# Performance work log

Measured on AMD Instinct MI355X. Metric: run time of the kernel, lower is better.

The kernel has to match this reference:

```python
import jax, jax.numpy as jnp
import numpy as np

N_E, N_U, N_D = 512, 256, 256
N_A = 16
N_FB = 4
N_SV = 256
N_PV = 64
D_IN0 = 3 * (4 * N_A) + 2 * 4   # 200, fb_block output at layer 0
D_IN = 3 * N_SV + 2 * N_PV      # 896, fb_block output thereafter


def _fb_block(s_v, p_v):
    # s_v: (n_e, d_s); p_v: (n_e, n_e, d_p)
    n_e = N_U + N_D
    su_m = jnp.tile(s_v[:N_U].mean(0)[None, :], (n_e, 1))
    sd_m = jnp.tile(s_v[N_U:].mean(0)[None, :], (n_e, 1))
    pu_m = p_v[:N_U].mean(0)   # (n_e, d_p)
    pd_m = p_v[N_U:].mean(0)
    return jnp.concatenate([su_m, sd_m, pu_m, pd_m, s_v], axis=-1)


def setup_inputs() -> dict:
    key = jax.random.key(0)
    ks = jax.random.split(key, 16)

    def lin(k, fin, fout):
        k1, k2 = jax.random.split(k)
        lim = 1.0 / np.sqrt(fin)
        W = jax.random.uniform(k1, (fin, fout), minval=-lim, maxval=lim, dtype=jnp.float32)
        b = jax.random.uniform(k2, (fout,), minval=-lim, maxval=lim, dtype=jnp.float32)
        return W, b

    V0_W, V0_b = lin(ks[0], D_IN0, N_SV)
    W0_W, W0_b = lin(ks[1], 4, N_PV)
    VrW, Vrb, WrW, Wrb = [], [], [], []
    for i in range(N_FB - 1):
        w, b = lin(ks[2 + i], D_IN, N_SV); VrW.append(w); Vrb.append(b)
        w, b = lin(ks[6 + i], N_PV, N_PV); WrW.append(w); Wrb.append(b)
    Vr_W, Vr_b = jnp.stack(VrW), jnp.stack(Vrb)
    Wr_W, Wr_b = jnp.stack(WrW), jnp.stack(Wrb)
    Vhu_W, Vhu_b = lin(ks[10], D_IN, N_SV)
    Vhd_W, Vhd_b = lin(ks[11], D_IN, N_SV)
    wu_W, wu_b = lin(ks[12], N_SV, N_U)
    wd_W, wd_b = lin(ks[13], N_SV, N_D)
    r = jax.random.normal(ks[14], (N_E, 3), dtype=jnp.float32)
    a = jax.random.normal(ks[15], (N_A, 3), dtype=jnp.float32) * 2.0
    return dict(r=r, a=a, V0_W=V0_W, V0_b=V0_b, Vr_W=Vr_W, Vr_b=Vr_b,
                W0_W=W0_W, W0_b=W0_b, Wr_W=Wr_W, Wr_b=Wr_b,
                Vhu_W=Vhu_W, Vhu_b=Vhu_b, Vhd_W=Vhd_W, Vhd_b=Vhd_b,
                wu_W=wu_W, wu_b=wu_b, wd_W=wd_W, wd_b=wd_b)


def reference(r, a, V0_W, V0_b, Vr_W, Vr_b, W0_W, W0_b, Wr_W, Wr_b,
              Vhu_W, Vhu_b, Vhd_W, Vhd_b, wu_W, wu_b, wd_W, wd_b):
    n_e = N_E
    eye = jnp.eye(n_e, dtype=r.dtype)[:, :, None]
    ra = r[:, None, :] - a[None, :, :]                       # (n_e, n_a, 3)
    ra_len = jnp.linalg.norm(ra, axis=-1, keepdims=True)
    rr = r[None, :, :] - r[:, None, :]                       # (n_e, n_e, 3)
    rr_len = jnp.linalg.norm(rr + eye, axis=-1, keepdims=True)
    s_v = jnp.concatenate([ra, ra_len], axis=-1).reshape(n_e, -1)   # (n_e, 4*n_a)
    p_v = jnp.concatenate([rr, rr_len], axis=-1)                    # (n_e, n_e, 4)
    s_blk = _fb_block(s_v, p_v)
    for l in range(N_FB):
        VW, Vb = (V0_W, V0_b) if l == 0 else (Vr_W[l - 1], Vr_b[l - 1])
        WW, Wb = (W0_W, W0_b) if l == 0 else (Wr_W[l - 1], Wr_b[l - 1])
        s_new = jnp.tanh(s_blk @ VW + Vb)
        s_v = s_new + s_v if s_v.shape[-1] == N_SV else s_new   # residual skips layer 0
        p_new = jnp.tanh(p_v @ WW + Wb)
        p_v = p_new + p_v if p_v.shape[-1] == N_PV else p_new
        s_blk = _fb_block(s_v, p_v)
    s_u = jnp.tanh(s_blk[:N_U] @ Vhu_W + Vhu_b)
    s_d = jnp.tanh(s_blk[N_U:] @ Vhd_W + Vhd_b)
    s_wu = s_u @ wu_W + wu_b                                  # (n_u, n_u)
    s_wd = s_d @ wd_W + wd_b                                  # (n_d, n_d)
    exp_u = jnp.linalg.norm(ra[:N_U], axis=-1, keepdims=True)  # (n_u, n_a, 1)
    exp_d = jnp.linalg.norm(ra[N_U:], axis=-1, keepdims=True)
    orb_u = (s_wu * jnp.exp(-exp_u).sum(axis=1))[None]         # (1, n_u, n_u)
    orb_d = (s_wd * jnp.exp(-exp_d).sum(axis=1))[None]
    # logabssumdet with n_det == 1, matrix dim > 1
    sgn_u, log_u = jnp.linalg.slogdet(orb_u)
    sgn_d, log_d = jnp.linalg.slogdet(orb_d)
    psi = (sgn_u * sgn_d * jnp.exp(log_u + log_d)).sum()
    return jnp.log(jnp.abs(psi))
```

## Files before the change

### kernel.cpp

```cpp
#include <hip/hip_runtime.h>
#include <hip/hip_bf16.h>

#define NE 512

__device__ __align__(16) float g_sv0[NE*64];
__device__ __align__(16) float g_sv[2][NE*256];
__device__ __align__(16) float g_pu4[NE*4];
__device__ __align__(16) float g_pd4[NE*4];
__device__ __align__(16) float g_puL[4*NE*64];
__device__ __align__(16) float g_pdL[4*NE*64];
__device__ __align__(16) float g_su0[64];
__device__ __align__(16) float g_sd0[64];
__device__ __align__(16) float g_su[256];
__device__ __align__(16) float g_sd[256];
__device__ __align__(16) float g_part4[4*16*NE*64];
__device__ __align__(16) float g_f[NE];
__device__ __align__(16) float g_hu[256*256];
__device__ __align__(16) float g_hd[256*256];
__device__ __align__(16) float g_orbu[256*256];
__device__ __align__(16) float g_orbd[256*256];
__device__ float g_logs[2];

__device__ __forceinline__ float tanh_fast(float x) {
  float e = __expf(2.f * x);
  return 1.f - 2.f / (e + 1.f);
}

__global__ __launch_bounds__(256, 2) void k_front(const float* __restrict__ r,
                                                  const float* __restrict__ a,
                                                  const float* __restrict__ W0,
                                                  const float* __restrict__ b0,
                                                  const float* __restrict__ Wr,
                                                  const float* __restrict__ brs) {
  __shared__ __align__(16) float xrow[4*32*68];
  __shared__ __align__(16) float wtile[4096];
  __shared__ __align__(16) float msc[4*4*68];
  __shared__ float red[4][4];
  int bid = blockIdx.x, t = threadIdx.x;
  if (bid < 512) {
    int j = bid;
    if (j == 0) {
      for (int h = 0; h < 2; ++h) {
        int e = h*256 + t;
        float rx = r[3*e], ry = r[3*e+1], rz = r[3*e+2];
        float facc = 0.f;
        #pragma unroll
        for (int at = 0; at < 16; ++at) {
          float dx = rx - a[3*at], dy = ry - a[3*at+1], dz = rz - a[3*at+2];
          float len = sqrtf(dx*dx + dy*dy + dz*dz);
          g_sv0[e*64 + 4*at + 0] = dx;
          g_sv0[e*64 + 4*at + 1] = dy;
          g_sv0[e*64 + 4*at + 2] = dz;
          g_sv0[e*64 + 4*at + 3] = len;
          facc += expf(-len);
        }
        g_f[e] = facc;
      }
      __syncthreads();
      if (t < 128) {
        int h = t >> 6, c = t & 63;
        float s = 0.f;
        for (int i = 0; i < 256; ++i) s += g_sv0[(h*256 + i)*64 + c];
        (h ? g_sd0 : g_su0)[c] = s * (1.f/256.f);
      }
      __syncthreads();
    }
    float rjx = r[3*j], rjy = r[3*j+1], rjz = r[3*j+2];
    for (int h = 0; h < 2; ++h) {
      int i = h*256 + t;
      float dx = rjx - r[3*i], dy = rjy - r[3*i+1], dz = rjz - r[3*i+2];
      float ee = (i == j) ? 1.f : 0.f;
      float ex = dx+ee, ey = dy+ee, ez = dz+ee;
      float len = sqrtf(ex*ex + ey*ey + ez*ez);
      float v0 = dx, v1 = dy, v2 = dz, v3 = len;
      #pragma unroll
      for (int m = 1; m < 64; m <<= 1) {
        v0 += __shfl_xor(v0, m); v1 += __shfl_xor(v1, m);
        v2 += __shfl_xor(v2, m); v3 += __shfl_xor(v3, m);
      }
      if ((t & 63) == 0) {
        int wv = t >> 6;
        red[wv][0]=v0; red[wv][1]=v1; red[wv][2]=v2; red[wv][3]=v3;
      }
      __syncthreads();
      if (t == 0) {
        float* dst = h ? g_pd4 : g_pu4;
        #pragma unroll
        for (int c = 0; c < 4; ++c)
          dst[j*4 + c] = (red[0][c]+red[1][c]+red[2][c]+red[3][c]) * (1.f/256.f);
      }
      __syncthreads();
    }
  } else {
    int lane = t & 63, wv = t >> 6;
    int gw = (bid - 512)*4 + wv;
    int j = gw >> 4, chunk = gw & 15;
    int i0 = chunk * 32;
    int rg = lane >> 4, cg = lane & 15;
    float* xr = xrow + wv*(32*68);
    float* ms = msc + wv*(4*68);
    float rjx = r[3*j], rjy = r[3*j+1], rjz = r[3*j+2];
    float xres[8][4];
    {
      float4 w0 = *(const float4*)&W0[0*64 + 4*cg];
      float4 w1 = *(const float4*)&W0[1*64 + 4*cg];
      float4 w2 = *(const float4*)&W0[2*64 + 4*cg];
      float4 w3 = *(const float4*)&W0[3*64 + 4*cg];
      float4 bv = *(const float4*)&b0[4*cg];
      #pragma unroll
      for (int q = 0; q < 8; ++q) {
        int row = 4*q + rg;
        int i = i0 + row;
        float dx = rjx - r[3*i], dy = rjy - r[3*i+1], dz = rjz - r[3*i+2];
        float ee = (i == j) ? 1.f : 0.f;
        float ex = dx+ee, ey = dy+ee, ez = dz+ee;
        float len = sqrtf(ex*ex + ey*ey + ez*ez);
        float y0 = tanh_fast(bv.x + dx*w0.x + dy*w1.x + dz*w2.x + len*w3.x);
        float y1 = tanh_fast(bv.y + dx*w0.y + dy*w1.y + dz*w2.y + len*w3.y);
        float y2 = tanh_fast(bv.z + dx*w0.z + dy*w1.z + dz*w2.z + len*w3.z);
        float y3 = tanh_fast(bv.w + dx*w0.w + dy*w1.w + dz*w2.w + len*w3.w);
        xres[q][0]=y0; xres[q][1]=y1; xres[q][2]=y2; xres[q][3]=y3;
        float4 yv; yv.x=y0; yv.y=y1; yv.z=y2; yv.w=y3;
        *(float4*)&xr[row*68 + 4*cg] = yv;
      }
      float cs0=0,cs1=0,cs2=0,cs3=0;
      #pragma unroll
      for (int q=0;q<8;++q){cs0+=xres[q][0];cs1+=xres[q][1];cs2+=xres[q][2];cs3+=xres[q][3];}
      ms[rg*68+4*cg+0]=cs0; ms[rg*68+4*cg+1]=cs1;
      ms[rg*68+4*cg+2]=cs2; ms[rg*68+4*cg+3]=cs3;
      float tot = ms[0*68+lane]+ms[1*68+lane]+ms[2*68+lane]+ms[3*68+lane];
      g_part4[0*(16*NE*64) + chunk*(NE*64) + j*64 + lane] = tot;
    }
    for (int l = 0; l < 3; ++l) {
      __syncthreads();
      for (int idx = t; idx < 4096; idx += 256) wtile[idx] = Wr[l*4096 + idx];
      __syncthreads();
      float4 bv = *(const float4*)&brs[l*64 + 4*cg];
      float acc[8][4];
      #pragma unroll
      for (int q=0;q<8;++q){acc[q][0]=bv.x;acc[q][1]=bv.y;acc[q][2]=bv.z;acc[q][3]=bv.w;}
      #pragma unroll 4
      for (int kq = 0; kq < 16; ++kq) {
        float4 wv0 = *(const float4*)&wtile[(4*kq+0)*64 + 4*cg];
        float4 wv1 = *(const float4*)&wtile[(4*kq+1)*64 + 4*cg];
        float4 wv2 = *(const float4*)&wtile[(4*kq+2)*64 + 4*cg];
        float4 wv3 = *(const float4*)&wtile[(4*kq+3)*64 + 4*cg];
        #pragma unroll
        for (int q = 0; q < 8; ++q) {
          float4 xv = *(const float4*)&xr[(4*q+rg)*68 + 4*kq];
          acc[q][0] += xv.x*wv0.x + xv.y*wv1.x + xv.z*wv2.x + xv.w*wv3.x;
          acc[q][1] += xv.x*wv0.y + xv.y*wv1.y + xv.z*wv2.y + xv.w*wv3.y;
          acc[q][2] += xv.x*wv0.z + xv.y*wv1.z + xv.z*wv2.z + xv.w*wv3.z;
          acc[q][3] += xv.x*wv0.w + xv.y*wv1.w + xv.z*wv2.w + xv.w*wv3.w;
        }
      }
      float cs0=0,cs1=0,cs2=0,cs3=0;
      #pragma unroll
      for (int q = 0; q < 8; ++q) {
        float y0 = tanh_fast(acc[q][0]) + xres[q][0];
        float y1 = tanh_fast(acc[q][1]) + xres[q][1];
        float y2 = tanh_fast(acc[q][2]) + xres[q][2];
        float y3 = tanh_fast(acc[q][3]) + xres[q][3];
        xres[q][0]=y0; xres[q][1]=y1; xres[q][2]=y2; xres[q][3]=y3;
        float4 yv; yv.x=y0; yv.y=y1; yv.z=y2; yv.w=y3;
        *(float4*)&xr[(4*q+rg)*68 + 4*cg] = yv;
        cs0+=y0; cs1+=y1; cs2+=y2; cs3+=y3;
      }
      ms[rg*68+4*cg+0]=cs0; ms[rg*68+4*cg+1]=cs1;
      ms[rg*68+4*cg+2]=cs2; ms[rg*68+4*cg+3]=cs3;
      float tot = ms[0*68+lane]+ms[1*68+lane]+ms[2*68+lane]+ms[3*68+lane];
      g_part4[(l+1)*(16*NE*64) + chunk*(NE*64) + j*64 + lane] = tot;
    }
  }
}

__global__ __launch_bounds__(256) void k_reduce_p() {
  int idx = blockIdx.x*256 + threadIdx.x;
  int l = idx >> 16;
  int rem = idx & 65535;
  int half = rem >> 15;
  int r2 = rem & 32767;
  int j = r2 >> 6, c = r2 & 63;
  const float* pp = g_part4 + l*(16*NE*64) + half*(8*NE*64) + j*64 + c;
  float s = 0.f;
  #pragma unroll
  for (int ch = 0; ch < 8; ++ch) s += pp[ch*(NE*64)];
  (half ? g_pdL : g_puL)[l*(NE*64) + j*64 + c] = s * (1.f/256.f);
}

__global__ __launch_bounds__(256) void k_smean(int svsel) {
  int h = blockIdx.x, t = threadIdx.x;
  const float* sv = g_sv[svsel];
  float s = 0.f;
  for (int i = 0; i < 256; ++i) s += sv[(h*256 + i)*256 + t];
  (h ? g_sd : g_su)[t] = s * (1.f/256.f);
}

template<int PUK, int SVK, int MEANK>
__global__ __launch_bounds__(256) void k_smm(int which, const float* __restrict__ W,
                                             const float* __restrict__ Wb,
                                             const float* __restrict__ W2,
                                             const float* __restrict__ Wb2,
                                             int pl) {
  constexpr int MAINK = 2*PUK + SVK;
  __shared__ __align__(16) float wsl[MAINK*32];
  __shared__ float insl[32*(MAINK+1)];
  __shared__ float biasv[32];
  __shared__ float bred[256];
  const float *pu_p=nullptr, *pd_p=nullptr, *sv_p=nullptr, *su_p=nullptr, *sd_p=nullptr;
  const float *res_p=nullptr, *rs_p=nullptr;
  float* out_p = nullptr;
  int t = threadIdx.x;
  int rg = blockIdx.x, cg = blockIdx.y;
  int grp = 0, rgl = rg;
  if (which >= 4) { grp = rg >> 3; rgl = rg & 7; }
  const float* Wsel = (which >= 4 && grp) ? W2 : W;
  const float* Wbsel = (which >= 4 && grp) ? Wb2 : Wb;
  int in_base = 0, dotanh = 1;
  switch (which) {
    case 0: pu_p=g_pu4; pd_p=g_pd4; su_p=g_su0; sd_p=g_sd0; sv_p=g_sv0;
            out_p=g_sv[0]; in_base=rg*32; break;
    case 1: case 2: case 3:
      pu_p=g_puL + pl*(NE*64); pd_p=g_pdL + pl*(NE*64); su_p=g_su; sd_p=g_sd;
      sv_p=g_sv[(which+1)&1]; res_p=sv_p; out_p=g_sv[which&1]; in_base=rg*32; break;
    case 4: pu_p=g_puL + pl*(NE*64); pd_p=g_pdL + pl*(NE*64); su_p=g_su; sd_p=g_sd;
            sv_p=g_sv[1]; out_p = grp ? g_hd : g_hu; in_base = grp*256 + rgl*32; break;
    default: sv_p = grp ? g_hd : g_hu; out_p = grp ? g_orbd : g_orbu;
             rs_p = g_f + grp*256; in_base = rgl*32; dotanh = 0; break;
  }
  int out_base = (which >= 4) ? rgl*32 : rg*32;
  int col0 = cg * 32;
  for (int idx = t; idx < MAINK*32; idx += 256) {
    int c = idx >> 5, cl = idx & 31;
    wsl[idx] = Wsel[(2*MEANK + c)*256 + col0 + cl];
  }
  for (int rr = 0; rr < 32; ++rr) {
    int row = in_base + rr;
    for (int c = t; c < MAINK; c += 256) {
      float v;
      if (c < PUK) v = pu_p[row*PUK + c];
      else if (c < 2*PUK) v = pd_p[row*PUK + (c - PUK)];
      else v = sv_p[row*SVK + (c - 2*PUK)];
      insl[rr*(MAINK+1) + c] = v;
    }
  }
  {
    int pcol = t & 31, ps = t >> 5;
    float bacc = 0.f;
    if (MEANK > 0) {
      for (int c = ps; c < MEANK; c += 8)
        bacc += su_p[c]*Wsel[c*256 + col0 + pcol] + sd_p[c]*Wsel[(MEANK + c)*256 + col0 + pcol];
    }
    bred[ps*32 + pcol] = bacc;
  }
  __syncthreads();
  if (t < 32) {
    float s = Wbsel[col0 + t];
    #pragma unroll
    for (int p8 = 0; p8 < 8; ++p8) s += bred[p8*32 + t];
    biasv[t] = s;
  }
  __syncthreads();
  int c4 = t & 7, rl = t >> 3;
  float a0 = biasv[4*c4], a1 = biasv[4*c4+1], a2 = biasv[4*c4+2], a3 = biasv[4*c4+3];
  const float* inrow = &insl[rl*(MAINK+1)];
  #pragma unroll 4
  for (int c = 0; c < MAINK; ++c) {
    float iv = inrow[c];
    float4 wv = *(const float4*)&wsl[c*32 + 4*c4];
    a0 += iv*wv.x; a1 += iv*wv.y; a2 += iv*wv.z; a3 += iv*wv.w;
  }
  int rowA = out_base + rl;
  int col = col0 + 4*c4;
  if (dotanh) { a0=tanh_fast(a0); a1=tanh_fast(a1); a2=tanh_fast(a2); a3=tanh_fast(a3); }
  if (res_p) {
    float4 rv = *(const float4*)&res_p[rowA*256 + col];
    a0 += rv.x; a1 += rv.y; a2 += rv.z; a3 += rv.w;
  }
  if (rs_p) { float fsc = rs_p[rowA]; a0*=fsc; a1*=fsc; a2*=fsc; a3*=fsc; }
  float4 ov; ov.x=a0; ov.y=a1; ov.z=a2; ov.w=a3;
  *(float4*)&out_p[rowA*256 + col] = ov;
}

#define REP8(M) M(0) M(1) M(2) M(3) M(4) M(5) M(6) M(7)
#define DPPMAX(v, CTRL) { unsigned _o = (unsigned)__builtin_amdgcn_update_dpp(0, (int)(v), CTRL, 0xf, 0xf, true); \
                          (v) = (v) > _o ? (v) : _o; }

__global__ __launch_bounds__(512, 2) void k_lu() {
  __shared__ __align__(16) float colbuf[2][256];
  __shared__ __align__(16) float prowbuf[2][16*20];
  const float* A = (blockIdx.x == 0) ? g_orbu : g_orbd;
  int t = threadIdx.x;
  int tile_c = t >> 5;
  int tile_r = t & 31;
  int lane = t & 63;
  int br = tile_r * 8;
  int pb = tile_c * 20;
  const float4* Ap = (const float4*)(A + br*256 + tile_c*16);
#define DECLROW(R) float4 M##R##_0 = Ap[R*64+0], M##R##_1 = Ap[R*64+1], \
                          M##R##_2 = Ap[R*64+2], M##R##_3 = Ap[R*64+3];
  REP8(DECLROW)
#undef DECLROW
  unsigned um = 0;
  if (tile_c == 0) {
#define INIT0(R) colbuf[0][br+R] = M##R##_0.x;
    REP8(INIT0)
#undef INIT0
  }
  __syncthreads();
  float prod = 1.f;
  int esum = 0;
  float m0=0,m1=0,m2=0,m3=0,m4=0,m5=0,m6=0,m7=0;
  for (int k = 0; k < 256; ++k) {
    const float* cbin = colbuf[k & 1];
    float4 cv = *(const float4*)&cbin[4*lane];
    float4 ca = *(const float4*)&cbin[br];
    float4 cb2 = *(const float4*)&cbin[br+4];
    bool aliveU = (tile_c*16 + 15) >= k;
    if (k > 0 && aliveU) {
      const float* pwp = &prowbuf[(k-1) & 1][pb];
      float4 P0 = *(const float4*)&pwp[0];
      float4 P1 = *(const float4*)&pwp[4];
      float4 P2 = *(const float4*)&pwp[8];
      float4 P3 = *(const float4*)&pwp[12];
#define UPD(R) { float mr = m##R; \
  M##R##_0.x -= mr*P0.x; M##R##_0.y -= mr*P0.y; M##R##_0.z -= mr*P0.z; M##R##_0.w -= mr*P0.w; \
  M##R##_1.x -= mr*P1.x; M##R##_1.y -= mr*P1.y; M##R##_1.z -= mr*P1.z; M##R##_1.w -= mr*P1.w; \
  M##R##_2.x -= mr*P2.x; M##R##_2.y -= mr*P2.y; M##R##_2.z -= mr*P2.z; M##R##_2.w -= mr*P2.w; \
  M##R##_3.x -= mr*P3.x; M##R##_3.y -= mr*P3.y; M##R##_3.z -= mr*P3.z; M##R##_3.w -= mr*P3.w; }
      REP8(UPD)
#undef UPD
    }
    unsigned b0 = (um & 1u) ? 0u : ((__float_as_uint(fabsf(cv.x)) & 0xFFFFFF00u) | (unsigned)(4*lane+0));
    unsigned b1 = (um & 2u) ? 0u : ((__float_as_uint(fabsf(cv.y)) & 0xFFFFFF00u) | (unsigned)(4*lane+1));
    unsigned b2 = (um & 4u) ? 0u : ((__float_as_uint(fabsf(cv.z)) & 0xFFFFFF00u) | (unsigned)(4*lane+2));
    unsigned b3 = (um & 8u) ? 0u : ((__float_as_uint(fabsf(cv.w)) & 0xFFFFFF00u) | (unsigned)(4*lane+3));
    unsigned bb = max(max(b0,b1), max(b2,b3));
    DPPMAX(bb, 0x111) DPPMAX(bb, 0x112) DPPMAX(bb, 0x114) DPPMAX(bb, 0x118)
    DPPMAX(bb, 0x142) DPPMAX(bb, 0x143)
    bb = (unsigned)__builtin_amdgcn_readlane((int)bb, 63);
    int p = (int)(bb & 255u);
    int wl = p >> 2, cc = p & 3;
    unsigned px = (unsigned)__builtin_amdgcn_readlane((int)__float_as_uint(cv.x), wl);
    unsigned py = (unsigned)__builtin_amdgcn_readlane((int)__float_as_uint(cv.y), wl);
    unsigned pz = (unsigned)__builtin_amdgcn_readlane((int)__float_as_uint(cv.z), wl);
    unsigned pw = (unsigned)__builtin_amdgcn_readlane((int)__float_as_uint(cv.w), wl);
    float piv = __uint_as_float(cc==0 ? px : cc==1 ? py : cc==2 ? pz : pw);
    int ee; float mant = frexpf(fabsf(piv), &ee);
    prod *= mant; esum += ee;
    int e2; prod = frexpf(prod, &e2); esum += e2;
    if (wl == lane) um |= 1u << cc;
    if (k == 255) break;
    float rp = 1.0f / piv;
    m0 = ca.x*rp; m1 = ca.y*rp; m2 = ca.z*rp; m3 = ca.w*rp;
    m4 = cb2.x*rp; m5 = cb2.y*rp; m6 = cb2.z*rp; m7 = cb2.w*rp;
    bool aliveK = (tile_c*16 + 15) > k;
    if (aliveK && tile_r == (p >> 3)) {
      float* pw_ = &prowbuf[k & 1][pb];
      switch (p & 7) {
#define PUBC(R) case R: *(float4*)&pw_[0] = M##R##_0; *(float4*)&pw_[4] = M##R##_1; \
                        *(float4*)&pw_[8] = M##R##_2; *(float4*)&pw_[12] = M##R##_3; break;
        REP8(PUBC)
#undef PUBC
      }
    }
    int kn = k + 1;
    if (tile_c == (kn >> 4)) {
      float e0,e1,e2b,e3,e4,e5,e6,e7;
      switch (kn & 15) {
#define EXTC(I, G, C) case I: e0=M0_##G.C; e1=M1_##G.C; e2b=M2_##G.C; e3=M3_##G.C; \
                              e4=M4_##G.C; e5=M5_##G.C; e6=M6_##G.C; e7=M7_##G.C; break;
        EXTC(0,0,x) EXTC(1,0,y) EXTC(2,0,z) EXTC(3,0,w)
        EXTC(4,1,x) EXTC(5,1,y) EXTC(6,1,z) EXTC(7,1,w)
        EXTC(8,2,x) EXTC(9,2,y) EXTC(10,2,z) EXTC(11,2,w)
        EXTC(12,3,x) EXTC(13,3,y) EXTC(14,3,z) EXTC(15,3,w)
#undef EXTC
      }
      float sel;
      switch (p & 7) {
        case 0: sel = e0; break; case 1: sel = e1; break;
        case 2: sel = e2b; break; case 3: sel = e3; break;
        case 4: sel = e4; break; case 5: sel = e5; break;
        case 6: sel = e6; break; default: sel = e7; break;
      }
      float pv = __shfl(sel, (tile_c & 1)*32 + (p >> 3), 64);
      float4 w0, w1;
      w0.x = e0 - m0*pv; w0.y = e1 - m1*pv; w0.z = e2b - m2*pv; w0.w = e3 - m3*pv;
      w1.x = e4 - m4*pv; w1.y = e5 - m5*pv; w1.z = e6 - m6*pv; w1.w = e7 - m7*pv;
      *(float4*)&colbuf[kn & 1][br] = w0;
      *(float4*)&colbuf[kn & 1][br+4] = w1;
    }
    __syncthreads();
  }
  if (t == 0) g_logs[blockIdx.x] = logf(prod) + (float)esum * 0.69314718055994531f;
}

__global__ void k_final(float* out) { out[0] = g_logs[0] + g_logs[1]; }

extern "C" void kernel_launch(void* const* d_in, const int* in_sizes, int n_in,
                              void* d_out, int out_size, void* d_ws, size_t ws_size,
                              hipStream_t stream) {
  const float* r     = (const float*)d_in[0];
  const float* a     = (const float*)d_in[1];
  const float* V0_W  = (const float*)d_in[2];
  const float* V0_b  = (const float*)d_in[3];
  const float* Vr_W  = (const float*)d_in[4];
  const float* Vr_b  = (const float*)d_in[5];
  const float* W0_W  = (const float*)d_in[6];
  const float* W0_b  = (const float*)d_in[7];
  const float* Wr_W  = (const float*)d_in[8];
  const float* Wr_b  = (const float*)d_in[9];
  const float* Vhu_W = (const float*)d_in[10];
  const float* Vhu_b = (const float*)d_in[11];
  const float* Vhd_W = (const float*)d_in[12];
  const float* Vhd_b = (const float*)d_in[13];
  const float* wu_W  = (const float*)d_in[14];
  const float* wu_b  = (const float*)d_in[15];
  const float* wd_W  = (const float*)d_in[16];
  const float* wd_b  = (const float*)d_in[17];
  float* out = (float*)d_out;

  k_front<<<2560, 256, 0, stream>>>(r, a, W0_W, W0_b, Wr_W, Wr_b);
  k_reduce_p<<<1024, 256, 0, stream>>>();

  k_smm<4,64,64><<<dim3(16,8), 256, 0, stream>>>(0, V0_W, V0_b, nullptr, nullptr, 0);
  k_smean<<<2, 256, 0, stream>>>(0);
  k_smm<64,256,256><<<dim3(16,8), 256, 0, stream>>>(1, Vr_W + 0*896*256, Vr_b + 0,
                                                    nullptr, nullptr, 0);
  k_smean<<<2, 256, 0, stream>>>(1);
  k_smm<64,256,256><<<dim3(16,8), 256, 0, stream>>>(2, Vr_W + 1*896*256, Vr_b + 256,
                                                    nullptr, nullptr, 1);
  k_smean<<<2, 256, 0, stream>>>(0);
  k_smm<64,256,256><<<dim3(16,8), 256, 0, stream>>>(3, Vr_W + 2*896*256, Vr_b + 512,
                                                    nullptr, nullptr, 2);
  k_smean<<<2, 256, 0, stream>>>(1);
  k_smm<64,256,256><<<dim3(16,8), 256, 0, stream>>>(4, Vhu_W, Vhu_b, Vhd_W, Vhd_b, 3);
  k_smm<0,256,0><<<dim3(16,8), 256, 0, stream>>>(6, wu_W, wu_b, wd_W, wd_b, 0);
  k_lu<<<2, 512, 0, stream>>>();
  k_final<<<1, 1, 0, stream>>>(out);
}
```

Measured before the change: 641.8 us.

## Fuse mid-stage kernels into one persistent kernel with software grid barriers

Replaces the reduce, smean and smm launches with a single persistent 256-block kernel that moves between stages using an atomic-counter grid barrier. The matmul tiles are halved to 16 rows so 256 blocks fill more CUs, and the K loop is split across two thread halves that reduce through shared memory. The separate final-sum kernel is folded into the LU kernel using an atomic completion counter. This removes many small launches and their gaps, but correctness now depends on all 256 blocks being co-resident, and every barrier spin-waits on global atomics.

```diff
diff --git a/kernel.cpp b/kernel.cpp
--- a/kernel.cpp
+++ b/kernel.cpp
@@ -20,6 +20,8 @@
 __device__ __align__(16) float g_orbu[256*256];
 __device__ __align__(16) float g_orbd[256*256];
 __device__ float g_logs[2];
+__device__ unsigned g_barcnt;
+__device__ unsigned g_ludone;
 
 __device__ __forceinline__ float tanh_fast(float x) {
   float e = __expf(2.f * x);
@@ -37,6 +39,7 @@
   __shared__ __align__(16) float msc[4*4*68];
   __shared__ float red[4][4];
   int bid = blockIdx.x, t = threadIdx.x;
+  if (bid == 0 && t == 0) { g_barcnt = 0u; g_ludone = 0u; }
   if (bid < 512) {
     int j = bid;
     if (j == 0) {
@@ -174,119 +177,181 @@
   }
 }
 
-__global__ __launch_bounds__(256) void k_reduce_p() {
-  int idx = blockIdx.x*256 + threadIdx.x;
-  int l = idx >> 16;
-  int rem = idx & 65535;
-  int half = rem >> 15;
-  int r2 = rem & 32767;
-  int j = r2 >> 6, c = r2 & 63;
-  const float* pp = g_part4 + l*(16*NE*64) + half*(8*NE*64) + j*64 + c;
-  float s = 0.f;
-  #pragma unroll
-  for (int ch = 0; ch < 8; ++ch) s += pp[ch*(NE*64)];
-  (half ? g_pdL : g_puL)[l*(NE*64) + j*64 + c] = s * (1.f/256.f);
-}
-
-__global__ __launch_bounds__(256) void k_smean(int svsel) {
-  int h = blockIdx.x, t = threadIdx.x;
-  const float* sv = g_sv[svsel];
-  float s = 0.f;
-  for (int i = 0; i < 256; ++i) s += sv[(h*256 + i)*256 + t];
-  (h ? g_sd : g_su)[t] = s * (1.f/256.f);
-}
-
-template<int PUK, int SVK, int MEANK>
-__global__ __launch_bounds__(256) void k_smm(int which, const float* __restrict__ W,
-                                             const float* __restrict__ Wb,
-                                             const float* __restrict__ W2,
-                                             const float* __restrict__ Wb2,
-                                             int pl) {
-  constexpr int MAINK = 2*PUK + SVK;
-  __shared__ __align__(16) float wsl[MAINK*32];
-  __shared__ float insl[32*(MAINK+1)];
-  __shared__ float biasv[32];
-  __shared__ float bred[256];
-  const float *pu_p=nullptr, *pd_p=nullptr, *sv_p=nullptr, *su_p=nullptr, *sd_p=nullptr;
-  const float *res_p=nullptr, *rs_p=nullptr;
-  float* out_p = nullptr;
-  int t = threadIdx.x;
-  int rg = blockIdx.x, cg = blockIdx.y;
-  int grp = 0, rgl = rg;
-  if (which >= 4) { grp = rg >> 3; rgl = rg & 7; }
-  const float* Wsel = (which >= 4 && grp) ? W2 : W;
-  const float* Wbsel = (which >= 4 && grp) ? Wb2 : Wb;
-  int in_base = 0, dotanh = 1;
-  switch (which) {
-    case 0: pu_p=g_pu4; pd_p=g_pd4; su_p=g_su0; sd_p=g_sd0; sv_p=g_sv0;
-            out_p=g_sv[0]; in_base=rg*32; break;
-    case 1: case 2: case 3:
-      pu_p=g_puL + pl*(NE*64); pd_p=g_pdL + pl*(NE*64); su_p=g_su; sd_p=g_sd;
-      sv_p=g_sv[(which+1)&1]; res_p=sv_p; out_p=g_sv[which&1]; in_base=rg*32; break;
-    case 4: pu_p=g_puL + pl*(NE*64); pd_p=g_pdL + pl*(NE*64); su_p=g_su; sd_p=g_sd;
-            sv_p=g_sv[1]; out_p = grp ? g_hd : g_hu; in_base = grp*256 + rgl*32; break;
-    default: sv_p = grp ? g_hd : g_hu; out_p = grp ? g_orbd : g_orbu;
-             rs_p = g_f + grp*256; in_base = rgl*32; dotanh = 0; break;
-  }
-  int out_base = (which >= 4) ? rgl*32 : rg*32;
-  int col0 = cg * 32;
+__device__ __forceinline__ void gridbar(int t, int phase) {
+  __syncthreads();
+  if (t == 0) {
+    __hip_atomic_fetch_add(&g_barcnt, 1u, __ATOMIC_ACQ_REL, __HIP_MEMORY_SCOPE_AGENT);
+    unsigned tgt = 256u * (unsigned)phase;
+    while (__hip_atomic_load(&g_barcnt, __ATOMIC_ACQUIRE, __HIP_MEMORY_SCOPE_AGENT) < tgt)
+      __builtin_amdgcn_s_sleep(2);
+  }
+  __syncthreads();
+}
+
+__device__ __forceinline__ void smm_stage(int bid, int t,
+    const float* W, const float* Wb,
+    const float* pu_p, const float* pd_p,
+    const float* su_p, const float* sd_p,
+    const float* sv_p, const float* res_p, const float* rs_p,
+    float* out_p, int PUK, int SVK, int MAINK, int MEANK,
+    int sin_base, int out_base, bool dotanh,
+    float* wsl, float* insl, float* bred, float* biasv, float4* pacc) {
+  int cg = bid & 7, col0 = cg*32;
   for (int idx = t; idx < MAINK*32; idx += 256) {
     int c = idx >> 5, cl = idx & 31;
-    wsl[idx] = Wsel[(2*MEANK + c)*256 + col0 + cl];
-  }
-  for (int rr = 0; rr < 32; ++rr) {
-    int row = in_base + rr;
+    wsl[idx] = W[(2*MEANK + c)*256 + col0 + cl];
+  }
+  for (int rr = 0; rr < 16; ++rr) {
+    int row = sin_base + rr;
     for (int c = t; c < MAINK; c += 256) {
       float v;
       if (c < PUK) v = pu_p[row*PUK + c];
       else if (c < 2*PUK) v = pd_p[row*PUK + (c - PUK)];
       else v = sv_p[row*SVK + (c - 2*PUK)];
-      insl[rr*(MAINK+1) + c] = v;
+      insl[rr*385 + c] = v;
     }
   }
   {
     int pcol = t & 31, ps = t >> 5;
     float bacc = 0.f;
+    for (int c = ps; c < MEANK; c += 8)
+      bacc += su_p[c]*W[c*256 + col0 + pcol] + sd_p[c]*W[(MEANK + c)*256 + col0 + pcol];
+    bred[ps*32 + pcol] = bacc;
+  }
+  __syncthreads();
+  if (t < 32) {
+    float s = Wb[col0 + t];
     if (MEANK > 0) {
-      for (int c = ps; c < MEANK; c += 8)
-        bacc += su_p[c]*Wsel[c*256 + col0 + pcol] + sd_p[c]*Wsel[(MEANK + c)*256 + col0 + pcol];
-    }
-    bred[ps*32 + pcol] = bacc;
-  }
-  __syncthreads();
-  if (t < 32) {
-    float s = Wbsel[col0 + t];
-    #pragma unroll
-    for (int p8 = 0; p8 < 8; ++p8) s += bred[p8*32 + t];
+      #pragma unroll
+      for (int p8 = 0; p8 < 8; ++p8) s += bred[p8*32 + t];
+    }
     biasv[t] = s;
   }
   __syncthreads();
-  int c4 = t & 7, rl = t >> 3;
-  float a0 = biasv[4*c4], a1 = biasv[4*c4+1], a2 = biasv[4*c4+2], a3 = biasv[4*c4+3];
-  const float* inrow = &insl[rl*(MAINK+1)];
+  int kh = t >> 7, tt = t & 127, rl = tt >> 3, c4 = tt & 7;
+  int H = MAINK >> 1, c0 = kh*H;
+  float a0=0.f, a1=0.f, a2=0.f, a3=0.f;
+  const float* inrow = &insl[rl*385];
   #pragma unroll 4
-  for (int c = 0; c < MAINK; ++c) {
+  for (int c = c0; c < c0 + H; ++c) {
     float iv = inrow[c];
     float4 wv = *(const float4*)&wsl[c*32 + 4*c4];
     a0 += iv*wv.x; a1 += iv*wv.y; a2 += iv*wv.z; a3 += iv*wv.w;
   }
-  int rowA = out_base + rl;
-  int col = col0 + 4*c4;
-  if (dotanh) { a0=tanh_fast(a0); a1=tanh_fast(a1); a2=tanh_fast(a2); a3=tanh_fast(a3); }
-  if (res_p) {
-    float4 rv = *(const float4*)&res_p[rowA*256 + col];
-    a0 += rv.x; a1 += rv.y; a2 += rv.z; a3 += rv.w;
-  }
-  if (rs_p) { float fsc = rs_p[rowA]; a0*=fsc; a1*=fsc; a2*=fsc; a3*=fsc; }
-  float4 ov; ov.x=a0; ov.y=a1; ov.z=a2; ov.w=a3;
-  *(float4*)&out_p[rowA*256 + col] = ov;
+  float4 av; av.x=a0; av.y=a1; av.z=a2; av.w=a3;
+  pacc[t] = av;
+  __syncthreads();
+  if (kh == 0) {
+    float4 o = pacc[t + 128];
+    a0 += o.x + biasv[4*c4+0];
+    a1 += o.y + biasv[4*c4+1];
+    a2 += o.z + biasv[4*c4+2];
+    a3 += o.w + biasv[4*c4+3];
+    if (dotanh) { a0=tanh_fast(a0); a1=tanh_fast(a1); a2=tanh_fast(a2); a3=tanh_fast(a3); }
+    int rowA = out_base + rl;
+    int col = col0 + 4*c4;
+    if (res_p) {
+      float4 rv = *(const float4*)&res_p[rowA*256 + col];
+      a0 += rv.x; a1 += rv.y; a2 += rv.z; a3 += rv.w;
+    }
+    if (rs_p) { float fsc = rs_p[rowA]; a0*=fsc; a1*=fsc; a2*=fsc; a3*=fsc; }
+    float4 ov; ov.x=a0; ov.y=a1; ov.z=a2; ov.w=a3;
+    *(float4*)&out_p[rowA*256 + col] = ov;
+  }
+}
+
+__device__ __forceinline__ void smean_stage(int bid, int t, const float* sv, float* bred) {
+  if (bid < 16) {
+    int h = bid & 1, cs = bid >> 1;
+    int pcol = t & 31, rseg = t >> 5;
+    float s = 0.f;
+    for (int i = rseg*32; i < rseg*32 + 32; ++i)
+      s += sv[(h*256 + i)*256 + cs*32 + pcol];
+    bred[rseg*32 + pcol] = s;
+    __syncthreads();
+    if (t < 32) {
+      float tot = 0.f;
+      #pragma unroll
+      for (int r8 = 0; r8 < 8; ++r8) tot += bred[r8*32 + t];
+      (h ? g_sd : g_su)[cs*32 + t] = tot * (1.f/256.f);
+    }
+  }
+}
+
+__global__ __launch_bounds__(256) void k_mid(const float* __restrict__ V0_W,
+                                             const float* __restrict__ V0_b,
+                                             const float* __restrict__ Vr_W,
+                                             const float* __restrict__ Vr_b,
+                                             const float* __restrict__ Vhu_W,
+                                             const float* __restrict__ Vhu_b,
+                                             const float* __restrict__ Vhd_W,
+                                             const float* __restrict__ Vhd_b,
+                                             const float* __restrict__ wu_W,
+                                             const float* __restrict__ wu_b,
+                                             const float* __restrict__ wd_W,
+                                             const float* __restrict__ wd_b) {
+  __shared__ __align__(16) float wsl[384*32];
+  __shared__ __align__(16) float insl[16*385];
+  __shared__ float bred[256];
+  __shared__ float biasv[32];
+  __shared__ __align__(16) float4 pacc[256];
+  int bid = blockIdx.x, t = threadIdx.x;
+  #pragma unroll
+  for (int rep = 0; rep < 4; ++rep) {
+    int idx = rep*65536 + bid*256 + t;
+    int l = idx >> 16;
+    int rem = idx & 65535;
+    int half = rem >> 15;
+    int r2 = rem & 32767;
+    const float* pp = g_part4 + l*(16*NE*64) + half*(8*NE*64) + r2;
+    float s = 0.f;
+    #pragma unroll
+    for (int ch = 0; ch < 8; ++ch) s += pp[ch*(NE*64)];
+    (half ? g_pdL : g_puL)[l*(NE*64) + r2] = s * (1.f/256.f);
+  }
+  gridbar(t, 1);
+  int rg = bid >> 3;
+  int grp = rg >> 4, rgl = rg & 15;
+  smm_stage(bid, t, V0_W, V0_b, g_pu4, g_pd4, g_su0, g_sd0, g_sv0,
+            nullptr, nullptr, g_sv[0], 4, 64, 72, 64, rg*16, rg*16, true,
+            wsl, insl, bred, biasv, pacc);
+  gridbar(t, 2);
+  smean_stage(bid, t, g_sv[0], bred);
+  gridbar(t, 3);
+  smm_stage(bid, t, Vr_W + 0*896*256, Vr_b + 0, g_puL + 0*(NE*64), g_pdL + 0*(NE*64),
+            g_su, g_sd, g_sv[0], g_sv[0], nullptr, g_sv[1], 64, 256, 384, 256,
+            rg*16, rg*16, true, wsl, insl, bred, biasv, pacc);
+  gridbar(t, 4);
+  smean_stage(bid, t, g_sv[1], bred);
+  gridbar(t, 5);
+  smm_stage(bid, t, Vr_W + 1*896*256, Vr_b + 256, g_puL + 1*(NE*64), g_pdL + 1*(NE*64),
+            g_su, g_sd, g_sv[1], g_sv[1], nullptr, g_sv[0], 64, 256, 384, 256,
+            rg*16, rg*16, true, wsl, insl, bred, biasv, pacc);
+  gridbar(t, 6);
+  smean_stage(bid, t, g_sv[0], bred);
+  gridbar(t, 7);
+  smm_stage(bid, t, Vr_W + 2*896*256, Vr_b + 512, g_puL + 2*(NE*64), g_pdL + 2*(NE*64),
+            g_su, g_sd, g_sv[0], g_sv[0], nullptr, g_sv[1], 64, 256, 384, 256,
+            rg*16, rg*16, true, wsl, insl, bred, biasv, pacc);
+  gridbar(t, 8);
+  smean_stage(bid, t, g_sv[1], bred);
+  gridbar(t, 9);
+  smm_stage(bid, t, grp ? Vhd_W : Vhu_W, grp ? Vhd_b : Vhu_b,
+            g_puL + 3*(NE*64), g_pdL + 3*(NE*64), g_su, g_sd, g_sv[1],
+            nullptr, nullptr, grp ? g_hd : g_hu, 64, 256, 384, 256,
+            grp*256 + rgl*16, rgl*16, true, wsl, insl, bred, biasv, pacc);
+  gridbar(t, 10);
+  smm_stage(bid, t, grp ? wd_W : wu_W, grp ? wd_b : wu_b,
+            nullptr, nullptr, nullptr, nullptr, grp ? g_hd : g_hu,
+            nullptr, g_f + grp*256, grp ? g_orbd : g_orbu, 0, 256, 256, 0,
+            rgl*16, rgl*16, false, wsl, insl, bred, biasv, pacc);
 }
 
 #define REP8(M) M(0) M(1) M(2) M(3) M(4) M(5) M(6) M(7)
 #define DPPMAX(v, CTRL) { unsigned _o = (unsigned)__builtin_amdgcn_update_dpp(0, (int)(v), CTRL, 0xf, 0xf, true); \
                           (v) = (v) > _o ? (v) : _o; }
 
-__global__ __launch_bounds__(512, 2) void k_lu() {
+__global__ __launch_bounds__(512, 2) void k_lu(float* __restrict__ out) {
   __shared__ __align__(16) float colbuf[2][256];
   __shared__ __align__(16) float prowbuf[2][16*20];
   const float* A = (blockIdx.x == 0) ? g_orbu : g_orbd;
@@ -392,10 +457,17 @@
     }
     __syncthreads();
   }
-  if (t == 0) g_logs[blockIdx.x] = logf(prod) + (float)esum * 0.69314718055994531f;
-}
-
-__global__ void k_final(float* out) { out[0] = g_logs[0] + g_logs[1]; }
+  if (t == 0) {
+    float ls = logf(prod) + (float)esum * 0.69314718055994531f;
+    __hip_atomic_store(&g_logs[blockIdx.x], ls, __ATOMIC_RELEASE, __HIP_MEMORY_SCOPE_AGENT);
+    unsigned old = __hip_atomic_fetch_add(&g_ludone, 1u, __ATOMIC_ACQ_REL, __HIP_MEMORY_SCOPE_AGENT);
+    if (old == 1u) {
+      float l0 = __hip_atomic_load(&g_logs[0], __ATOMIC_ACQUIRE, __HIP_MEMORY_SCOPE_AGENT);
+      float l1 = __hip_atomic_load(&g_logs[1], __ATOMIC_ACQUIRE, __HIP_MEMORY_SCOPE_AGENT);
+      out[0] = l0 + l1;
+    }
+  }
+}
 
 extern "C" void kernel_launch(void* const* d_in, const int* in_sizes, int n_in,
                               void* d_out, int out_size, void* d_ws, size_t ws_size,
@@ -421,21 +493,7 @@
   float* out = (float*)d_out;
 
   k_front<<<2560, 256, 0, stream>>>(r, a, W0_W, W0_b, Wr_W, Wr_b);
-  k_reduce_p<<<1024, 256, 0, stream>>>();
-
-  k_smm<4,64,64><<<dim3(16,8), 256, 0, stream>>>(0, V0_W, V0_b, nullptr, nullptr, 0);
-  k_smean<<<2, 256, 0, stream>>>(0);
-  k_smm<64,256,256><<<dim3(16,8), 256, 0, stream>>>(1, Vr_W + 0*896*256, Vr_b + 0,
-                                                    nullptr, nullptr, 0);
-  k_smean<<<2, 256, 0, stream>>>(1);
-  k_smm<64,256,256><<<dim3(16,8), 256, 0, stream>>>(2, Vr_W + 1*896*256, Vr_b + 256,
-                                                    nullptr, nullptr, 1);
-  k_smean<<<2, 256, 0, stream>>>(0);
-  k_smm<64,256,256><<<dim3(16,8), 256, 0, stream>>>(3, Vr_W + 2*896*256, Vr_b + 512,
-                                                    nullptr, nullptr, 2);
-  k_smean<<<2, 256, 0, stream>>>(1);
-  k_smm<64,256,256><<<dim3(16,8), 256, 0, stream>>>(4, Vhu_W, Vhu_b, Vhd_W, Vhd_b, 3);
-  k_smm<0,256,0><<<dim3(16,8), 256, 0, stream>>>(6, wu_W, wu_b, wd_W, wd_b, 0);
-  k_lu<<<2, 512, 0, stream>>>();
-  k_final<<<1, 1, 0, stream>>>(out);
-}
+  k_mid<<<256, 256, 0, stream>>>(V0_W, V0_b, Vr_W, Vr_b, Vhu_W, Vhu_b,
+                                 Vhd_W, Vhd_b, wu_W, wu_b, wd_W, wd_b);
+  k_lu<<<2, 512, 0, stream>>>(out);
+}
```

Result: slower. 704.3 us (+9.7%).

## Fuse s-mean reduction into matmul epilogues and fold final sum into LU

Applied to the files above, without the earlier changes.

Removes the separate k_smean kernels. Each k_smm block now writes per-rowgroup column partial sums of its output, and the next layer's k_smm reduces those partials into shared memory before it starts. The k_final launch is also removed: the two LU blocks combine their log values through an atomic counter that is reset in k_front. This cuts several small serial kernel launches, including the 256-iteration column-mean loops, at the cost of a little redundant partial-sum reduction in every block.

```diff
diff --git a/kernel.cpp b/kernel.cpp
--- a/kernel.cpp
+++ b/kernel.cpp
@@ -11,15 +11,15 @@
 __device__ __align__(16) float g_pdL[4*NE*64];
 __device__ __align__(16) float g_su0[64];
 __device__ __align__(16) float g_sd0[64];
-__device__ __align__(16) float g_su[256];
-__device__ __align__(16) float g_sd[256];
 __device__ __align__(16) float g_part4[4*16*NE*64];
+__device__ __align__(16) float g_spart[2][16*256];
 __device__ __align__(16) float g_f[NE];
 __device__ __align__(16) float g_hu[256*256];
 __device__ __align__(16) float g_hd[256*256];
 __device__ __align__(16) float g_orbu[256*256];
 __device__ __align__(16) float g_orbd[256*256];
 __device__ float g_logs[2];
+__device__ unsigned g_ludone;
 
 __device__ __forceinline__ float tanh_fast(float x) {
   float e = __expf(2.f * x);
@@ -37,6 +37,7 @@
   __shared__ __align__(16) float msc[4*4*68];
   __shared__ float red[4][4];
   int bid = blockIdx.x, t = threadIdx.x;
+  if (bid == 0 && t == 0) g_ludone = 0u;
   if (bid < 512) {
     int j = bid;
     if (j == 0) {
@@ -180,20 +181,11 @@
   int rem = idx & 65535;
   int half = rem >> 15;
   int r2 = rem & 32767;
-  int j = r2 >> 6, c = r2 & 63;
-  const float* pp = g_part4 + l*(16*NE*64) + half*(8*NE*64) + j*64 + c;
+  const float* pp = g_part4 + l*(16*NE*64) + half*(8*NE*64) + r2;
   float s = 0.f;
   #pragma unroll
   for (int ch = 0; ch < 8; ++ch) s += pp[ch*(NE*64)];
-  (half ? g_pdL : g_puL)[l*(NE*64) + j*64 + c] = s * (1.f/256.f);
-}
-
-__global__ __launch_bounds__(256) void k_smean(int svsel) {
-  int h = blockIdx.x, t = threadIdx.x;
-  const float* sv = g_sv[svsel];
-  float s = 0.f;
-  for (int i = 0; i < 256; ++i) s += sv[(h*256 + i)*256 + t];
-  (h ? g_sd : g_su)[t] = s * (1.f/256.f);
+  (half ? g_pdL : g_puL)[l*(NE*64) + r2] = s * (1.f/256.f);
 }
 
 template<int PUK, int SVK, int MEANK>
@@ -201,12 +193,14 @@
                                              const float* __restrict__ Wb,
                                              const float* __restrict__ W2,
                                              const float* __restrict__ Wb2,
-                                             int pl) {
+                                             int pl, int rsp, int wsp) {
   constexpr int MAINK = 2*PUK + SVK;
   __shared__ __align__(16) float wsl[MAINK*32];
   __shared__ float insl[32*(MAINK+1)];
   __shared__ float biasv[32];
   __shared__ float bred[256];
+  __shared__ float susd[512];
+  __shared__ float wred[4][8][4];
   const float *pu_p=nullptr, *pd_p=nullptr, *sv_p=nullptr, *su_p=nullptr, *sd_p=nullptr;
   const float *res_p=nullptr, *rs_p=nullptr;
   float* out_p = nullptr;
@@ -221,12 +215,24 @@
     case 0: pu_p=g_pu4; pd_p=g_pd4; su_p=g_su0; sd_p=g_sd0; sv_p=g_sv0;
             out_p=g_sv[0]; in_base=rg*32; break;
     case 1: case 2: case 3:
-      pu_p=g_puL + pl*(NE*64); pd_p=g_pdL + pl*(NE*64); su_p=g_su; sd_p=g_sd;
+      pu_p=g_puL + pl*(NE*64); pd_p=g_pdL + pl*(NE*64);
       sv_p=g_sv[(which+1)&1]; res_p=sv_p; out_p=g_sv[which&1]; in_base=rg*32; break;
-    case 4: pu_p=g_puL + pl*(NE*64); pd_p=g_pdL + pl*(NE*64); su_p=g_su; sd_p=g_sd;
+    case 4: pu_p=g_puL + pl*(NE*64); pd_p=g_pdL + pl*(NE*64);
             sv_p=g_sv[1]; out_p = grp ? g_hd : g_hu; in_base = grp*256 + rgl*32; break;
     default: sv_p = grp ? g_hd : g_hu; out_p = grp ? g_orbd : g_orbu;
              rs_p = g_f + grp*256; in_base = rgl*32; dotanh = 0; break;
+  }
+  if (rsp >= 0 && MEANK == 256) {
+    const float* sp = g_spart[rsp];
+    for (int e = t; e < 512; e += 256) {
+      int half = e >> 8, c = e & 255;
+      float s = 0.f;
+      #pragma unroll
+      for (int g8 = 0; g8 < 8; ++g8) s += sp[(half*8 + g8)*256 + c];
+      susd[e] = s * (1.f/256.f);
+    }
+    su_p = &susd[0]; sd_p = &susd[256];
+    __syncthreads();
   }
   int out_base = (which >= 4) ? rgl*32 : rg*32;
   int col0 = cg * 32;
@@ -280,13 +286,31 @@
   if (rs_p) { float fsc = rs_p[rowA]; a0*=fsc; a1*=fsc; a2*=fsc; a3*=fsc; }
   float4 ov; ov.x=a0; ov.y=a1; ov.z=a2; ov.w=a3;
   *(float4*)&out_p[rowA*256 + col] = ov;
+  if (wsp >= 0) {
+    int lane = t & 63, wv = t >> 6;
+    float s0=a0, s1=a1, s2=a2, s3=a3;
+    #pragma unroll
+    for (int m = 8; m < 64; m <<= 1) {
+      s0 += __shfl_xor(s0, m); s1 += __shfl_xor(s1, m);
+      s2 += __shfl_xor(s2, m); s3 += __shfl_xor(s3, m);
+    }
+    if ((lane >> 3) == 0) {
+      wred[wv][c4][0]=s0; wred[wv][c4][1]=s1; wred[wv][c4][2]=s2; wred[wv][c4][3]=s3;
+    }
+    __syncthreads();
+    if (t < 32) {
+      int cc4 = t >> 2, cc = t & 3;
+      float tot = wred[0][cc4][cc]+wred[1][cc4][cc]+wred[2][cc4][cc]+wred[3][cc4][cc];
+      g_spart[wsp][rg*256 + col0 + 4*cc4 + cc] = tot;
+    }
+  }
 }
 
 #define REP8(M) M(0) M(1) M(2) M(3) M(4) M(5) M(6) M(7)
 #define DPPMAX(v, CTRL) { unsigned _o = (unsigned)__builtin_amdgcn_update_dpp(0, (int)(v), CTRL, 0xf, 0xf, true); \
                           (v) = (v) > _o ? (v) : _o; }
 
-__global__ __launch_bounds__(512, 2) void k_lu() {
+__global__ __launch_bounds__(512, 2) void k_lu(float* __restrict__ out) {
   __shared__ __align__(16) float colbuf[2][256];
   __shared__ __align__(16) float prowbuf[2][16*20];
   const float* A = (blockIdx.x == 0) ? g_orbu : g_orbd;
@@ -392,10 +416,17 @@
     }
     __syncthreads();
   }
-  if (t == 0) g_logs[blockIdx.x] = logf(prod) + (float)esum * 0.69314718055994531f;
-}
-
-__global__ void k_final(float* out) { out[0] = g_logs[0] + g_logs[1]; }
+  if (t == 0) {
+    float ls = logf(prod) + (float)esum * 0.69314718055994531f;
+    __hip_atomic_store(&g_logs[blockIdx.x], ls, __ATOMIC_RELEASE, __HIP_MEMORY_SCOPE_AGENT);
+    unsigned old = __hip_atomic_fetch_add(&g_ludone, 1u, __ATOMIC_ACQ_REL, __HIP_MEMORY_SCOPE_AGENT);
+    if (old == 1u) {
+      float l0 = __hip_atomic_load(&g_logs[0], __ATOMIC_ACQUIRE, __HIP_MEMORY_SCOPE_AGENT);
+      float l1 = __hip_atomic_load(&g_logs[1], __ATOMIC_ACQUIRE, __HIP_MEMORY_SCOPE_AGENT);
+      out[0] = l0 + l1;
+    }
+  }
+}
 
 extern "C" void kernel_launch(void* const* d_in, const int* in_sizes, int n_in,
                               void* d_out, int out_size, void* d_ws, size_t ws_size,
@@ -422,20 +453,17 @@
 
   k_front<<<2560, 256, 0, stream>>>(r, a, W0_W, W0_b, Wr_W, Wr_b);
   k_reduce_p<<<1024, 256, 0, stream>>>();
-
-  k_smm<4,64,64><<<dim3(16,8), 256, 0, stream>>>(0, V0_W, V0_b, nullptr, nullptr, 0);
-  k_smean<<<2, 256, 0, stream>>>(0);
+  k_smm<4,64,64><<<dim3(16,8), 256, 0, stream>>>(0, V0_W, V0_b, nullptr, nullptr,
+                                                 0, -1, 0);
   k_smm<64,256,256><<<dim3(16,8), 256, 0, stream>>>(1, Vr_W + 0*896*256, Vr_b + 0,
-                                                    nullptr, nullptr, 0);
-  k_smean<<<2, 256, 0, stream>>>(1);
+                                                    nullptr, nullptr, 0, 0, 1);
   k_smm<64,256,256><<<dim3(16,8), 256, 0, stream>>>(2, Vr_W + 1*896*256, Vr_b + 256,
-                                                    nullptr, nullptr, 1);
-  k_smean<<<2, 256, 0, stream>>>(0);
+                                                    nullptr, nullptr, 1, 1, 0);
   k_smm<64,256,256><<<dim3(16,8), 256, 0, stream>>>(3, Vr_W + 2*896*256, Vr_b + 512,
-                                                    nullptr, nullptr, 2);
-  k_smean<<<2, 256, 0, stream>>>(1);
-  k_smm<64,256,256><<<dim3(16,8), 256, 0, stream>>>(4, Vhu_W, Vhu_b, Vhd_W, Vhd_b, 3);
-  k_smm<0,256,0><<<dim3(16,8), 256, 0, stream>>>(6, wu_W, wu_b, wd_W, wd_b, 0);
-  k_lu<<<2, 512, 0, stream>>>();
-  k_final<<<1, 1, 0, stream>>>(out);
-}
+                                                    nullptr, nullptr, 2, 0, 1);
+  k_smm<64,256,256><<<dim3(16,8), 256, 0, stream>>>(4, Vhu_W, Vhu_b, Vhd_W, Vhd_b,
+                                                    3, 1, -1);
+  k_smm<0,256,0><<<dim3(16,8), 256, 0, stream>>>(6, wu_W, wu_b, wd_W, wd_b,
+                                                 0, -1, -1);
+  k_lu<<<2, 512, 0, stream>>>(out);
+}
```

New measurement: 610.1 us. 1.05x faster.
